# Kernel tuning notes

Hardware: AMD Instinct MI355X
Metric: run time of the kernel (lower is better)

The kernel has to match this reference:

```python
import jax, jax.numpy as jnp
import numpy as np

# V:N:M sparsity config (n=2 kept of m=8 per vector-block; mask pattern [1,0,1,0,0,0,0,0])
M_BLK = 8
KEEP_OFFSETS = np.array([0, 2], dtype=np.int32)  # positions kept in each m-block
B, S, D_IN, D_OUT = 2, 8192, 4096, 4096
K_KEPT = D_IN // M_BLK * len(KEEP_OFFSETS)  # 1024


def _keep_idx():
    # column indices of the surviving weight entries (same for every output row)
    blocks = np.arange(D_IN // M_BLK, dtype=np.int32)[:, None] * M_BLK  # [D_IN/M,1]
    return jnp.asarray((blocks + KEEP_OFFSETS[None, :]).reshape(-1))   # [K_KEPT]


def setup_inputs() -> dict:
    key = jax.random.key(0)
    k1, k2, k3 = jax.random.split(key, 3)
    x = jax.random.normal(k1, (B, S, D_IN), dtype=jnp.float32)
    values = jax.random.normal(k2, (D_OUT, K_KEPT), dtype=jnp.float32) * 0.02
    bias = jax.random.normal(k3, (D_OUT,), dtype=jnp.float32) * 0.02
    return {"x": x, "values": values, "bias": bias}


def reference(x, values, bias):
    # Sparse SpMM: gather kept input features, dense GEMM with compressed values.
    # Equivalent to x @ (masked dense W).T + bias, without materializing W.
    keep = _keep_idx()               # [K_KEPT] int32, constant metadata
    xg = x[..., keep]                # [B,S,K_KEPT]
    out = jnp.einsum('bsk,nk->bsn', xg, values) + bias  # [B,S,D_OUT]
    return out
```

## Files before the change

### kernel.cpp

```cpp
#include <hip/hip_runtime.h>
#include <hip/hip_bf16.h>


#define M_TOTAL 16384
#define DIN     4096
#define KDIM    1024
#define NDIM    4096

typedef unsigned short u16;
typedef unsigned int   u32;
typedef __bf16 bf16x8 __attribute__((ext_vector_type(8)));
typedef float  f32x4  __attribute__((ext_vector_type(4)));

typedef const void __attribute__((address_space(1)))* gp_t;
typedef void __attribute__((address_space(3)))*       lp_t;

__device__ __forceinline__ u16 f2bf(float f) {
    u32 u = __float_as_uint(f);
    u += 0x7FFFu + ((u >> 16) & 1u);
    return (u16)(u >> 16);
}
__device__ __forceinline__ u32 pack2(float a, float b) {
    return (u32)f2bf(a) | ((u32)f2bf(b) << 16);
}

__global__ void prep_kernel(const float* __restrict__ x, uint4* __restrict__ xg4,
                            const float* __restrict__ vals, uint4* __restrict__ vb4) {
    const int tid = threadIdx.x;
    if (blockIdx.x < 2048) {
        int i = blockIdx.x * 256 + tid;
        const int stride = 2048 * 256;
#pragma unroll
        for (int it = 0; it < 4; ++it, i += stride) {
            const float* p = x + (size_t)i * 32;
            float4 a = *(const float4*)p;
            float4 b = *(const float4*)(p + 8);
            float4 c = *(const float4*)(p + 16);
            float4 d = *(const float4*)(p + 24);
            xg4[i] = make_uint4(pack2(a.x, a.z), pack2(b.x, b.z),
                                pack2(c.x, c.z), pack2(d.x, d.z));
        }
    } else {
        int i = (blockIdx.x - 2048) * 256 + tid;
        const int stride = 256 * 256;
#pragma unroll
        for (int it = 0; it < 8; ++it, i += stride) {
            const float* p = vals + (size_t)i * 8;
            float4 a = *(const float4*)p;
            float4 b = *(const float4*)(p + 4);
            vb4[i] = make_uint4(pack2(a.x, a.y), pack2(a.z, a.w),
                                pack2(b.x, b.y), pack2(b.z, b.w));
        }
    }
}


#define LDSA(d, kh) (((d) * 2 + (kh)) * 16384)
#define LDSB(d, kh) (65536 + ((d) * 2 + (kh)) * 16384)

#define LOADA(d, kh, mh) { _Pragma("unroll") \
    for (int m_ = 0; m_ < 4; ++m_) \
        af[m_] = *(const bf16x8*)(lds + LDSA(d, kh) + (wr * 8 + (mh) * 4 + m_) * 1024 + fl_off); }

#define LOADB(d, kh) { _Pragma("unroll") \
    for (int n_ = 0; n_ < 4; ++n_) \
        bfr[n_] = *(const bf16x8*)(lds + LDSB(d, kh) + (wc * 4 + n_) * 1024 + fl_off); }

#define MFMA16(mh) { \
    __builtin_amdgcn_s_setprio(1); \
    _Pragma("unroll") for (int m_ = 0; m_ < 4; ++m_) \
    _Pragma("unroll") for (int n_ = 0; n_ < 4; ++n_) \
        acc[(mh) * 4 + m_][n_] = __builtin_amdgcn_mfma_f32_16x16x32_bf16( \
            af[m_], bfr[n_], acc[(mh) * 4 + m_][n_], 0, 0, 0); \
    __builtin_amdgcn_s_setprio(0); }

#define BAR() __builtin_amdgcn_s_barrier()
#define VMCNT6() asm volatile("s_waitcnt vmcnt(6)" ::: "memory")

__global__ __launch_bounds__(512, 2) void gemm_kernel(
    const u16* __restrict__ A, const u16* __restrict__ Bv,
    const float* __restrict__ bias, float* __restrict__ C)
{
    __shared__ __align__(1024) char lds[131072];

    const int tid  = threadIdx.x;
    const int lane = tid & 63;
    const int wid  = tid >> 6;
    const int wr   = wid >> 2;
    const int wc   = wid & 3;
    const int lrow = lane & 15;
    const int lg   = lane >> 4;

    const int bb   = blockIdx.x;
    const int btm0 = (bb & 7) * 8 + (bb >> 7);
    const int btn  = (bb >> 3) & 15;

    const int st_r0 = wid * 16 + (lane >> 2);
    const int st_ck = ((lane & 3) * 8) ^ ((lane & 32) >> 1);
    const u16* A0  = A  + (size_t)(btm0 * 256 + st_r0) * KDIM + st_ck;
    const u16* Bs0 = Bv + (size_t)(btn  * 256 + st_r0) * KDIM + st_ck;
    const int dst0 = tid * 16;

    const int fl_off = lrow * 64 + ((lg * 16) ^ (((lrow >> 3) & 1) << 5));

    auto STAGE = [&](const u16* as_, int s) {
        const int kt = s >> 2, j = s & 3;
        const int d = kt & 1, kh = (j >> 1) & 1;
        const int ko = kt * 64 + kh * 32;
        const u16* src = (j & 1) ? Bs0 : as_;
        const int base = ((j & 1) ? 65536 : 0) + (d * 2 + kh) * 16384;
        __builtin_amdgcn_global_load_lds((gp_t)(src + ko),
            (lp_t)(lds + base + dst0), 16, 0, 0);
        __builtin_amdgcn_global_load_lds((gp_t)(src + 128 * KDIM + ko),
            (lp_t)(lds + base + 8192 + dst0), 16, 0, 0);
    };

    const int c_col0 = btn * 256 + wc * 64 + lrow;
    float bvr[4];
#pragma unroll
    for (int n = 0; n < 4; ++n) bvr[n] = bias[c_col0 + n * 16];

    f32x4 acc[8][4] = {};
    bf16x8 af[4], bfr[4];

    STAGE(A0, 0); STAGE(A0, 1); STAGE(A0, 2); STAGE(A0, 3);
    STAGE(A0, 4); STAGE(A0, 5); STAGE(A0, 6);
    VMCNT6();
    BAR();

#pragma unroll 1
    for (int r = 0; r < 4; ++r) {
        const u16* Ar = A0 + (size_t)r * 512 * KDIM;
        const u16* An = (r < 3) ? (Ar + 512 * KDIM) : Ar;

#pragma unroll 1
        for (int t = 0; t < 7; ++t) {
            const int s0 = 8 * t + 7;
            LOADB(0, 0); LOADA(0, 0, 0); STAGE(Ar, s0);     BAR(); MFMA16(0); BAR();
            LOADA(0, 0, 1);              STAGE(Ar, s0 + 1); BAR(); MFMA16(1); BAR();
            LOADB(0, 1); LOADA(0, 1, 0); STAGE(Ar, s0 + 2); BAR(); MFMA16(0); BAR();
            LOADA(0, 1, 1);              STAGE(Ar, s0 + 3); BAR(); MFMA16(1);
            VMCNT6(); BAR();
            LOADB(1, 0); LOADA(1, 0, 0); STAGE(Ar, s0 + 4); BAR(); MFMA16(0); BAR();
            LOADA(1, 0, 1);              STAGE(Ar, s0 + 5); BAR(); MFMA16(1); BAR();
            LOADB(1, 1); LOADA(1, 1, 0); STAGE(Ar, s0 + 6); BAR(); MFMA16(0); BAR();
            LOADA(1, 1, 1);              STAGE(Ar, s0 + 7); BAR(); MFMA16(1);
            VMCNT6(); BAR();
        }
        LOADB(0, 0); LOADA(0, 0, 0); STAGE(Ar, 63); BAR(); MFMA16(0); BAR();
        LOADA(0, 0, 1);              STAGE(An, 0);  BAR(); MFMA16(1); BAR();
        LOADB(0, 1); LOADA(0, 1, 0); STAGE(An, 1);  BAR(); MFMA16(0); BAR();
        LOADA(0, 1, 1);              STAGE(An, 2);  BAR(); MFMA16(1);
        VMCNT6(); BAR();
        LOADB(1, 0); LOADA(1, 0, 0); STAGE(An, 3);  BAR(); MFMA16(0); BAR();
        LOADA(1, 0, 1);              STAGE(An, 4);  BAR(); MFMA16(1); BAR();
        LOADB(1, 1); LOADA(1, 1, 0); STAGE(An, 5);  BAR(); MFMA16(0); BAR();
        LOADA(1, 1, 1);              STAGE(An, 6);  BAR(); MFMA16(1);
        VMCNT6(); BAR();

        const int c_row0 = (btm0 + 2 * r) * 256 + wr * 128 + lg * 4;
#pragma unroll
        for (int mi = 0; mi < 8; ++mi) {
            const int row = c_row0 + (mi >> 2) * 64 + (mi & 3) * 16;
#pragma unroll
            for (int n = 0; n < 4; ++n) {
#pragma unroll
                for (int j = 0; j < 4; ++j)
                    C[(size_t)(row + j) * NDIM + c_col0 + n * 16] = acc[mi][n][j] + bvr[n];
                acc[mi][n] = (f32x4){0.f, 0.f, 0.f, 0.f};
            }
        }
    }
}

extern "C" void kernel_launch(void* const* d_in, const int* in_sizes, int n_in,
                              void* d_out, int out_size, void* d_ws, size_t ws_size,
                              hipStream_t stream) {
    const float* x      = (const float*)d_in[0];
    const float* values = (const float*)d_in[1];
    const float* bias   = (const float*)d_in[2];
    float* out = (float*)d_out;

    u16* xg = (u16*)d_ws;
    u16* vb = (u16*)((char*)d_ws + ((size_t)32 << 20));

    prep_kernel<<<2304, 256, 0, stream>>>(x, (uint4*)xg, values, (uint4*)vb);
    gemm_kernel<<<256, 512, 0, stream>>>(xg, vb, bias, out);
}
```

Baseline: 226.4 us.

## Restructure GEMM staging into four-slot K ring buffer and regrid prep kernel

The GEMM main loop now uses a four-slot ring of 32-wide K chunks holding paired A and B tiles. Loads run three chunks ahead, with a uniform STEP macro and vmcnt(8) waits replacing the old double-buffer scheme and its vmcnt(6) waits. At the start of later rounds the wait is relaxed, since the prefetched slots were already in flight behind the epilogue stores. The prep kernel is regridded into more blocks, each thread doing less work, to raise memory-level parallelism for the bf16 gather and cast. The tighter in-flight accounting relies on in-order vmcnt counting that includes stores.

```diff
diff --git a/kernel.cpp b/kernel.cpp
--- a/kernel.cpp
+++ b/kernel.cpp
@@ -24,47 +24,40 @@
     return (u32)f2bf(a) | ((u32)f2bf(b) << 16);
 }
 
-__global__ void prep_kernel(const float* __restrict__ x, uint4* __restrict__ xg4,
+__global__ void prep_kernel(const float* __restrict__ x, uint2* __restrict__ xg2,
                             const float* __restrict__ vals, uint4* __restrict__ vb4) {
     const int tid = threadIdx.x;
-    if (blockIdx.x < 2048) {
+    if (blockIdx.x < 4096) {
         int i = blockIdx.x * 256 + tid;
-        const int stride = 2048 * 256;
+        const int stride = 4096 * 256;
 #pragma unroll
         for (int it = 0; it < 4; ++it, i += stride) {
-            const float* p = x + (size_t)i * 32;
-            float4 a = *(const float4*)p;
-            float4 b = *(const float4*)(p + 8);
-            float4 c = *(const float4*)(p + 16);
-            float4 d = *(const float4*)(p + 24);
-            xg4[i] = make_uint4(pack2(a.x, a.z), pack2(b.x, b.z),
-                                pack2(c.x, c.z), pack2(d.x, d.z));
+            const float* p = x + (size_t)i * 16;
+            float4 f0 = *(const float4*)p;
+            float4 f1 = *(const float4*)(p + 8);
+            xg2[i] = make_uint2(pack2(f0.x, f0.z), pack2(f1.x, f1.z));
         }
     } else {
-        int i = (blockIdx.x - 2048) * 256 + tid;
-        const int stride = 256 * 256;
-#pragma unroll
-        for (int it = 0; it < 8; ++it, i += stride) {
-            const float* p = vals + (size_t)i * 8;
-            float4 a = *(const float4*)p;
-            float4 b = *(const float4*)(p + 4);
-            vb4[i] = make_uint4(pack2(a.x, a.y), pack2(a.z, a.w),
-                                pack2(b.x, b.y), pack2(b.z, b.w));
-        }
+        const int i = (blockIdx.x - 4096) * 256 + tid;
+        const float* p = vals + (size_t)i * 8;
+        float4 a = *(const float4*)p;
+        float4 b = *(const float4*)(p + 4);
+        vb4[i] = make_uint4(pack2(a.x, a.y), pack2(a.z, a.w),
+                            pack2(b.x, b.y), pack2(b.z, b.w));
     }
 }
 
 
-#define LDSA(d, kh) (((d) * 2 + (kh)) * 16384)
-#define LDSB(d, kh) (65536 + ((d) * 2 + (kh)) * 16384)
+#define ABASE(bc) ((bc) * 32768)
+#define BBASE(bc) ((bc) * 32768 + 16384)
 
-#define LOADA(d, kh, mh) { _Pragma("unroll") \
+#define LOADA(bc, mh) { _Pragma("unroll") \
     for (int m_ = 0; m_ < 4; ++m_) \
-        af[m_] = *(const bf16x8*)(lds + LDSA(d, kh) + (wr * 8 + (mh) * 4 + m_) * 1024 + fl_off); }
+        af[m_] = *(const bf16x8*)(lds + ABASE(bc) + (wr * 8 + (mh) * 4 + m_) * 1024 + fl_off); }
 
-#define LOADB(d, kh) { _Pragma("unroll") \
+#define LOADB(bc) { _Pragma("unroll") \
     for (int n_ = 0; n_ < 4; ++n_) \
-        bfr[n_] = *(const bf16x8*)(lds + LDSB(d, kh) + (wc * 4 + n_) * 1024 + fl_off); }
+        bfr[n_] = *(const bf16x8*)(lds + BBASE(bc) + (wc * 4 + n_) * 1024 + fl_off); }
 
 #define MFMA16(mh) { \
     __builtin_amdgcn_s_setprio(1); \
@@ -74,8 +67,26 @@
             af[m_], bfr[n_], acc[(mh) * 4 + m_][n_], 0, 0, 0); \
     __builtin_amdgcn_s_setprio(0); }
 
+#define SA(bc, src, ko) { \
+    __builtin_amdgcn_global_load_lds((gp_t)((src) + (ko)), \
+        (lp_t)(lds + ABASE(bc) + dst0), 16, 0, 0); \
+    __builtin_amdgcn_global_load_lds((gp_t)((src) + 128 * KDIM + (ko)), \
+        (lp_t)(lds + ABASE(bc) + 8192 + dst0), 16, 0, 0); }
+
+#define SB(bc, ko) { \
+    __builtin_amdgcn_global_load_lds((gp_t)(Bs0 + (ko)), \
+        (lp_t)(lds + BBASE(bc) + dst0), 16, 0, 0); \
+    __builtin_amdgcn_global_load_lds((gp_t)(Bs0 + 128 * KDIM + (ko)), \
+        (lp_t)(lds + BBASE(bc) + 8192 + dst0), 16, 0, 0); }
+
 #define BAR() __builtin_amdgcn_s_barrier()
-#define VMCNT6() asm volatile("s_waitcnt vmcnt(6)" ::: "memory")
+#define VMCNT8()  asm volatile("s_waitcnt vmcnt(8)"  ::: "memory")
+#define VMCNT63() asm volatile("s_waitcnt vmcnt(63)" ::: "memory")
+#define W01 { if (r == 0) { VMCNT8(); } else { VMCNT63(); } }
+
+#define STEP(bc, SAx, SBx, W) { \
+    LOADB(bc); LOADA(bc, 0); SAx; BAR(); MFMA16(0); BAR(); \
+    LOADA(bc, 1); SBx; W; BAR(); MFMA16(1); BAR(); }
 
 __global__ __launch_bounds__(512, 2) void gemm_kernel(
     const u16* __restrict__ A, const u16* __restrict__ Bv,
@@ -103,18 +114,6 @@
 
     const int fl_off = lrow * 64 + ((lg * 16) ^ (((lrow >> 3) & 1) << 5));
 
-    auto STAGE = [&](const u16* as_, int s) {
-        const int kt = s >> 2, j = s & 3;
-        const int d = kt & 1, kh = (j >> 1) & 1;
-        const int ko = kt * 64 + kh * 32;
-        const u16* src = (j & 1) ? Bs0 : as_;
-        const int base = ((j & 1) ? 65536 : 0) + (d * 2 + kh) * 16384;
-        __builtin_amdgcn_global_load_lds((gp_t)(src + ko),
-            (lp_t)(lds + base + dst0), 16, 0, 0);
-        __builtin_amdgcn_global_load_lds((gp_t)(src + 128 * KDIM + ko),
-            (lp_t)(lds + base + 8192 + dst0), 16, 0, 0);
-    };
-
     const int c_col0 = btn * 256 + wc * 64 + lrow;
     float bvr[4];
 #pragma unroll
@@ -123,9 +122,10 @@
     f32x4 acc[8][4] = {};
     bf16x8 af[4], bfr[4];
 
-    STAGE(A0, 0); STAGE(A0, 1); STAGE(A0, 2); STAGE(A0, 3);
-    STAGE(A0, 4); STAGE(A0, 5); STAGE(A0, 6);
-    VMCNT6();
+    SA(0, A0, 0);   SB(0, 0);
+    SA(1, A0, 32);  SB(1, 32);
+    SA(2, A0, 64);  SB(2, 64);
+    VMCNT8();
     BAR();
 
 #pragma unroll 1
@@ -133,30 +133,24 @@
         const u16* Ar = A0 + (size_t)r * 512 * KDIM;
         const u16* An = (r < 3) ? (Ar + 512 * KDIM) : Ar;
 
+        STEP(0, SA(3, Ar, 96),  SB(3, 96),  W01);
+        STEP(1, SA(0, Ar, 128), SB(0, 128), W01);
+        STEP(2, SA(1, Ar, 160), SB(1, 160), VMCNT8());
+        STEP(3, SA(2, Ar, 192), SB(2, 192), VMCNT8());
+
 #pragma unroll 1
-        for (int t = 0; t < 7; ++t) {
-            const int s0 = 8 * t + 7;
-            LOADB(0, 0); LOADA(0, 0, 0); STAGE(Ar, s0);     BAR(); MFMA16(0); BAR();
-            LOADA(0, 0, 1);              STAGE(Ar, s0 + 1); BAR(); MFMA16(1); BAR();
-            LOADB(0, 1); LOADA(0, 1, 0); STAGE(Ar, s0 + 2); BAR(); MFMA16(0); BAR();
-            LOADA(0, 1, 1);              STAGE(Ar, s0 + 3); BAR(); MFMA16(1);
-            VMCNT6(); BAR();
-            LOADB(1, 0); LOADA(1, 0, 0); STAGE(Ar, s0 + 4); BAR(); MFMA16(0); BAR();
-            LOADA(1, 0, 1);              STAGE(Ar, s0 + 5); BAR(); MFMA16(1); BAR();
-            LOADB(1, 1); LOADA(1, 1, 0); STAGE(Ar, s0 + 6); BAR(); MFMA16(0); BAR();
-            LOADA(1, 1, 1);              STAGE(Ar, s0 + 7); BAR(); MFMA16(1);
-            VMCNT6(); BAR();
+        for (int u = 1; u < 7; ++u) {
+            const int ko = (4 * u + 3) * 32;
+            STEP(0, SA(3, Ar, ko),      SB(3, ko),      VMCNT8());
+            STEP(1, SA(0, Ar, ko + 32), SB(0, ko + 32), VMCNT8());
+            STEP(2, SA(1, Ar, ko + 64), SB(1, ko + 64), VMCNT8());
+            STEP(3, SA(2, Ar, ko + 96), SB(2, ko + 96), VMCNT8());
         }
-        LOADB(0, 0); LOADA(0, 0, 0); STAGE(Ar, 63); BAR(); MFMA16(0); BAR();
-        LOADA(0, 0, 1);              STAGE(An, 0);  BAR(); MFMA16(1); BAR();
-        LOADB(0, 1); LOADA(0, 1, 0); STAGE(An, 1);  BAR(); MFMA16(0); BAR();
-        LOADA(0, 1, 1);              STAGE(An, 2);  BAR(); MFMA16(1);
-        VMCNT6(); BAR();
-        LOADB(1, 0); LOADA(1, 0, 0); STAGE(An, 3);  BAR(); MFMA16(0); BAR();
-        LOADA(1, 0, 1);              STAGE(An, 4);  BAR(); MFMA16(1); BAR();
-        LOADB(1, 1); LOADA(1, 1, 0); STAGE(An, 5);  BAR(); MFMA16(0); BAR();
-        LOADA(1, 1, 1);              STAGE(An, 6);  BAR(); MFMA16(1);
-        VMCNT6(); BAR();
+
+        STEP(0, SA(3, Ar, 992), SB(3, 992), VMCNT8());
+        STEP(1, SA(0, An, 0),   SB(0, 0),   VMCNT8());
+        STEP(2, SA(1, An, 32),  SB(1, 32),  VMCNT8());
+        STEP(3, SA(2, An, 64),  SB(2, 64),  VMCNT8());
 
         const int c_row0 = (btm0 + 2 * r) * 256 + wr * 128 + lg * 4;
 #pragma unroll
@@ -184,6 +178,6 @@
     u16* xg = (u16*)d_ws;
     u16* vb = (u16*)((char*)d_ws + ((size_t)32 << 20));
 
-    prep_kernel<<<2304, 256, 0, stream>>>(x, (uint4*)xg, values, (uint4*)vb);
+    prep_kernel<<<6144, 256, 0, stream>>>(x, (uint2*)xg, values, (uint4*)vb);
     gemm_kernel<<<256, 512, 0, stream>>>(xg, vb, bias, out);
 }
```

New measurement: 244.6 us. +8.1%, slower.
